# Kernel tuning notes

Measured on AMD Instinct MI355X. Metric: run time of the kernel, lower is better.

The kernel has to match this reference:

```python
import jax, jax.numpy as jnp
import numpy as np

B, P, T = 32, 196, 64
E = H = A = 512
V = 32000
L = 2  # num_layers


def _p(key, shape, scale=0.05):
    return jax.random.normal(key, shape, dtype=jnp.float32) * scale


def setup_inputs() -> dict:
    key = jax.random.key(0)
    ks = jax.random.split(key, 24)
    inp = {
        "encoder_out": jax.random.normal(ks[0], (B, P, E), dtype=jnp.float32),
        "captions": jax.random.randint(ks[1], (B, T), 0, V, dtype=jnp.int32),
        # embedding table (also tied fc weight)
        "emb_W": _p(ks[2], (V, E)),
        "fc_b": jnp.zeros((V,), jnp.float32),
        # attention
        "W_enc": _p(ks[3], (E, A)), "b_enc": jnp.zeros((A,), jnp.float32),
        "W_dec": _p(ks[4], (H, A)), "b_dec": jnp.zeros((A,), jnp.float32),
        "W_full": _p(ks[5], (A, 1)), "b_full": jnp.zeros((1,), jnp.float32),
        # LSTM layer 0 (input = 2E), layer 1 (input = H); PyTorch gate order i,f,g,o
        "Wih0": _p(ks[6], (4 * H, 2 * E)), "Whh0": _p(ks[7], (4 * H, H)),
        "bih0": jnp.zeros((4 * H,), jnp.float32), "bhh0": jnp.zeros((4 * H,), jnp.float32),
        "Wih1": _p(ks[8], (4 * H, H)), "Whh1": _p(ks[9], (4 * H, H)),
        "bih1": jnp.zeros((4 * H,), jnp.float32), "bhh1": jnp.zeros((4 * H,), jnp.float32),
        # init hidden/cell projections
        "W_init_h": _p(ks[10], (E, H * L)), "b_init_h": jnp.zeros((H * L,), jnp.float32),
        "W_init_c": _p(ks[11], (E, H * L)), "b_init_c": jnp.zeros((H * L,), jnp.float32),
    }
    return inp


def _lstm_cell(x, h, c, Wih, Whh, b):
    gates = x @ Wih.T + h @ Whh.T + b  # [B, 4H]
    i, f, g, o = jnp.split(gates, 4, axis=-1)
    c_new = jax.nn.sigmoid(f) * c + jax.nn.sigmoid(i) * jnp.tanh(g)
    h_new = jax.nn.sigmoid(o) * jnp.tanh(c_new)
    return h_new, c_new


def _forward(encoder_out, captions, emb_W, fc_b, W_enc, b_enc, W_dec, b_dec,
             W_full, b_full, Wih0, Whh0, bih0, bhh0, Wih1, Whh1, bih1, bhh1,
             W_init_h, b_init_h, W_init_c, b_init_c):
    # dropout is identity (eval mode)
    Bsz = encoder_out.shape[0]
    mean_enc = encoder_out.mean(axis=1)  # [B, E]
    # PyTorch: .view(num_layers, B, -1) on a [B, H*L] tensor -> flat reshape
    h = (mean_enc @ W_init_h + b_init_h).reshape(L, Bsz, H)
    c = (mean_enc @ W_init_c + b_init_c).reshape(L, Bsz, H)

    enc_att = encoder_out @ W_enc + b_enc  # [B, P, A] (timestep-invariant, hoisted)
    embs = emb_W[captions]  # [B, T, E]
    b0 = bih0 + bhh0
    b1 = bih1 + bhh1

    def step(carry, emb_t):
        h, c = carry  # each [L, B, H]
        att2 = h[-1] @ W_dec + b_dec  # [B, A]
        e = (jax.nn.relu(enc_att + att2[:, None, :]) @ W_full)[..., 0] + b_full[0]  # [B, P]
        alpha = jax.nn.softmax(e, axis=1)
        context = jnp.einsum('bp,bpe->be', alpha, encoder_out)  # [B, E]
        x = jnp.concatenate([emb_t, context], axis=-1)  # [B, 2E]
        h0, c0 = _lstm_cell(x, h[0], c[0], Wih0, Whh0, b0)
        h1, c1 = _lstm_cell(h0, h[1], c[1], Wih1, Whh1, b1)
        out = h1 @ emb_W.T + fc_b  # tied-weight projection [B, V]
        return (jnp.stack([h0, h1]), jnp.stack([c0, c1])), out

    (_, _), outs = jax.lax.scan(step, (h, c), jnp.swapaxes(embs, 0, 1))
    return jnp.swapaxes(outs, 0, 1)  # [B, T, V]


def reference(encoder_out, captions, emb_W, fc_b, W_enc, b_enc, W_dec, b_dec,
              W_full, b_full, Wih0, Whh0, bih0, bhh0, Wih1, Whh1, bih1, bhh1,
              W_init_h, b_init_h, W_init_c, b_init_c):
    return _forward(encoder_out, captions, emb_W, fc_b, W_enc, b_enc, W_dec, b_dec,
                    W_full, b_full, Wih0, Whh0, bih0, bhh0, Wih1, Whh1, bih1, bhh1,
                    W_init_h, b_init_h, W_init_c, b_init_c)
```

## Files before the change

### kernel.cpp

```cpp
#include <hip/hip_runtime.h>

typedef unsigned short u16;
typedef __attribute__((ext_vector_type(4))) float f32x4;
typedef __attribute__((ext_vector_type(2))) float f32x2;
typedef __attribute__((ext_vector_type(8))) short short8;

#define B_ 32
#define P_ 196
#define T_ 64
#define V_ 32000
#define SLABF 17408

#define AT_LOAD(p)     __hip_atomic_load((p), __ATOMIC_RELAXED, __HIP_MEMORY_SCOPE_AGENT)
#define AT_STORE(p,v)  __hip_atomic_store((p), (v), __ATOMIC_RELAXED, __HIP_MEMORY_SCOPE_AGENT)

__device__ __forceinline__ u16 f2bf(float x){
  unsigned int u = __float_as_uint(x);
  u += 0x7FFFu + ((u >> 16) & 1u);
  return (u16)(u >> 16);
}
__device__ __forceinline__ float bf2f(u16 x){
  return __uint_as_float(((unsigned int)x) << 16);
}
__device__ __forceinline__ float sigf(float x){ return 1.0f/(1.0f + __expf(-x)); }
__device__ __forceinline__ float tanhfast(float x){
  float e = __expf(-2.0f*fabsf(x));
  float t = (1.0f - e)/(1.0f + e);
  return x >= 0.0f ? t : -t;
}


__global__ __launch_bounds__(256) void k_cvt_bf16(const float* __restrict__ s,
                                                  u16* __restrict__ d, int n8){
  int i = blockIdx.x*256 + threadIdx.x;
  if (i >= n8) return;
  const f32x4* sp = (const f32x4*)(s + (size_t)i*8);
  f32x4 a = sp[0], b = sp[1];
  short8 v;
#pragma unroll
  for (int j=0;j<4;++j){ v[j] = (short)f2bf(a[j]); v[4+j] = (short)f2bf(b[j]); }
  *(short8*)(d + (size_t)i*8) = v;
}

__global__ __launch_bounds__(256) void k_wencT(const float* __restrict__ W, u16* __restrict__ WT){
  int tid = threadIdx.x;
  int kc = tid & 63, a = blockIdx.x*4 + (tid >> 6);
  short8 v;
#pragma unroll
  for (int j=0;j<8;++j) v[j] = (short)f2bf(W[(kc*8+j)*512 + a]);
  *(short8*)(WT + a*512 + kc*8) = v;
}

__global__ __launch_bounds__(256) void k_mean(const float* __restrict__ enc, float* __restrict__ mean){
  int b = blockIdx.x, tid = threadIdx.x;
  f32x2 acc; acc.x = 0.f; acc.y = 0.f;
  for (int p=0;p<P_;++p){
    f32x2 v = *(const f32x2*)(enc + ((size_t)(b*P_+p))*512 + tid*2);
    acc.x += v.x; acc.y += v.y;
  }
  acc.x *= (1.0f/196.0f); acc.y *= (1.0f/196.0f);
  *(f32x2*)(mean + b*512 + tid*2) = acc;
}

__global__ __launch_bounds__(256) void k_init_state(const float* __restrict__ mean,
    const float* __restrict__ Wh, const float* __restrict__ bh,
    const float* __restrict__ Wc, const float* __restrict__ bc,
    float* __restrict__ h0, float* __restrict__ h1,
    float* __restrict__ c0, float* __restrict__ c1){
  int bid = blockIdx.x;
  int which = bid >> 7, r = (bid >> 2) & 31, jg = bid & 3;
  const float* W = which ? Wc : Wh;
  const float* bb = which ? bc : bh;
  __shared__ float m[512];
  for (int i=threadIdx.x; i<512; i+=256) m[i] = mean[r*512 + i];
  __syncthreads();
  int j = jg*256 + threadIdx.x;
  float acc = bb[j];
  for (int e=0;e<512;++e) acc += m[e]*W[e*1024 + j];
  int l = r >> 4;
  int bb2 = ((r & 15) << 1) | (j >> 9);
  int hh = j & 511;
  float* dst = which ? (l ? c1 : c0) : (l ? h1 : h0);
  dst[bb2*512 + hh] = acc;
}

__global__ __launch_bounds__(256) void k_fuse_w(const float* __restrict__ Wih0,
    const float* __restrict__ Whh0, const float* __restrict__ Wih1,
    const float* __restrict__ Whh1, float* __restrict__ W0f, float* __restrict__ W1f){
  int r = blockIdx.x, tid = threadIdx.x;
  if (r < 2048){
    for (int k=tid; k<1536; k+=256)
      W0f[(size_t)r*1536+k] = (k<1024) ? Wih0[(size_t)r*1024+k] : Whh0[(size_t)r*512 + (k-1024)];
  } else {
    int r1 = r - 2048;
    for (int k=tid; k<1024; k+=256)
      W1f[(size_t)r1*1024+k] = (k<512) ? Wih1[(size_t)r1*512+k] : Whh1[(size_t)r1*512 + (k-512)];
  }
}

#define LDAP 40
__global__ __launch_bounds__(256) void k_gemm_bf16(
    const u16* __restrict__ A, const u16* __restrict__ Bm,
    const float* __restrict__ bias, float* __restrict__ C, int N){
  __shared__ __align__(16) u16 As[128*LDAP];
  __shared__ __align__(16) u16 Bs[128*LDAP];
  int tid = threadIdx.x, l = tid & 63, w = tid >> 6;
  int m0 = blockIdx.x * 128, n0 = blockIdx.y * 128;
  int wm = w >> 1, wn = w & 1;
  f32x4 acc[4][4];
#pragma unroll
  for (int a=0;a<4;++a)
#pragma unroll
    for (int b=0;b<4;++b) acc[a][b] = (f32x4)0.0f;
  int srow = tid >> 2, schunk = tid & 3;
  const u16* gA = A + (size_t)(m0 + srow)*512 + schunk*8;
  const u16* gB = Bm + (size_t)(n0 + srow)*512 + schunk*8;
  int lr = l & 15, lk = (l >> 4) * 8;
  for (int k0 = 0; k0 < 512; k0 += 32){
    short8 va0 = *(const short8*)(gA + k0);
    short8 va1 = *(const short8*)(gA + (size_t)64*512 + k0);
    short8 vb0 = *(const short8*)(gB + k0);
    short8 vb1 = *(const short8*)(gB + (size_t)64*512 + k0);
    __syncthreads();
    *(short8*)(As + srow*LDAP + schunk*8) = va0;
    *(short8*)(As + (64+srow)*LDAP + schunk*8) = va1;
    *(short8*)(Bs + srow*LDAP + schunk*8) = vb0;
    *(short8*)(Bs + (64+srow)*LDAP + schunk*8) = vb1;
    __syncthreads();
    short8 af[4], bfv[4];
#pragma unroll
    for (int mt=0; mt<4; ++mt) af[mt]  = *(const short8*)(As + (wm*64 + mt*16 + lr)*LDAP + lk);
#pragma unroll
    for (int nt=0; nt<4; ++nt) bfv[nt] = *(const short8*)(Bs + (wn*64 + nt*16 + lr)*LDAP + lk);
#pragma unroll
    for (int mt=0; mt<4; ++mt)
#pragma unroll
      for (int nt=0; nt<4; ++nt)
        acc[mt][nt] = __builtin_amdgcn_mfma_f32_16x16x32_bf16(af[mt], bfv[nt], acc[mt][nt], 0, 0, 0);
  }
#pragma unroll
  for (int mt=0; mt<4; ++mt){
    int row = m0 + wm*64 + mt*16 + ((l >> 4) << 2);
#pragma unroll
    for (int nt=0; nt<4; ++nt){
      int col = n0 + wn*64 + nt*16 + (l & 15);
      float bv = bias[col];
#pragma unroll
      for (int j=0;j<4;++j)
        C[(size_t)(row + j)*N + col] = acc[mt][nt][j] + bv;
    }
  }
}


struct RA {
  const float* enc; const int* caps; const float* embW;
  const u16* WdecBF; const float* bdec; const float* Wfull; const float* bfull;
  const u16* encattBF; const float* W0f; const float* W1f;
  const float* bih0; const float* bhh0; const float* bih1; const float* bhh1;
  float* h0g; float* h1g; float* att2g; float* ctxg;
  const float* c0init; const float* c1init;
  u16* h1_all; int* slots; int* go;
};

__device__ __forceinline__ void gbar(int* slots, int* go, int gen){
  __syncthreads();
  if (blockIdx.x == 0){
    int tid = threadIdx.x;
    if (tid >= 1 && tid < 256){
      while (AT_LOAD(&slots[tid]) < gen) __builtin_amdgcn_s_sleep(1);
    }
    __syncthreads();
    if (tid == 0) AT_STORE(go, gen);
  } else {
    if (threadIdx.x == 0){
      AT_STORE(&slots[blockIdx.x], gen);
      while (AT_LOAD(go) < gen) __builtin_amdgcn_s_sleep(1);
    }
    __syncthreads();
  }
  asm volatile("" ::: "memory");
}

__global__ __launch_bounds__(512) void k_recur(RA a){
  int bid = blockIdx.x, tid = threadIdx.x;
  int lane = tid & 63, wv = tid >> 6;
  __shared__ __align__(16) float w0s[12288];
  __shared__ __align__(16) float w1s[8192];
  __shared__ float red[2048];
  __shared__ float c0s[64], c1s[64];
  __shared__ float SinvS;
  __shared__ int capl[32];

  int xcd = bid & 7;
  int ab = xcd*4 + ((bid >> 3) & 3);
  int as = bid >> 5, c0col = as*64;
  int bb = tid >> 4, ksg = tid & 15;

  for (int idx = tid; idx < 12288; idx += 512){
    int r = idx / 1536, rem = idx - r*1536;
    int ch = rem >> 9, rem2 = rem & 511;
    int q = rem2 >> 6, rem3 = rem2 & 63;
    int ks = rem3 >> 2, e = rem3 & 3;
    int grow = (r >> 1)*512 + bid*2 + (r & 1);
    w0s[idx] = a.W0f[(size_t)grow*1536 + ch*512 + ks*32 + q*4 + e];
  }
  for (int idx = tid; idx < 8192; idx += 512){
    int r = idx >> 10, rem = idx & 1023;
    int ch = rem >> 9, rem2 = rem & 511;
    int q = rem2 >> 6, rem3 = rem2 & 63;
    int ks = rem3 >> 2, e = rem3 & 3;
    int grow = (r >> 1)*512 + bid*2 + (r & 1);
    w1s[idx] = a.W1f[(size_t)grow*1024 + ch*512 + ks*32 + q*4 + e];
  }
  if (tid < 64){
    int ci = tid >> 5, b = tid & 31, cell = bid*2 + ci;
    c0s[ci*32+b] = a.c0init[b*512 + cell];
    c1s[ci*32+b] = a.c1init[b*512 + cell];
  }
  __syncthreads();

  for (int t = 0; t < T_; ++t){
    const float* h1_rd = a.h1g + (size_t)t*SLABF;
    const float* h0_rd = a.h0g + (size_t)t*SLABF;
    float*       h0_wr = a.h0g + (size_t)(t+1)*SLABF;
    float*       h1_wr = a.h1g + (size_t)(t+1)*SLABF;
    float*       at_wr = a.att2g + (size_t)t*SLABF;
    const float* at_rd = at_wr;
    float*       cx_wr = a.ctxg + (size_t)t*SLABF;
    const float* cx_rd = cx_wr;
    int genb = t*4;

    {
      float* h1s = red; float* gp = red + 512;
      h1s[tid] = h1_rd[ab*512 + tid];
      __syncthreads();
      int c = lane, ksx = wv;
      float accp = 0.f;
      const u16* wpd = a.WdecBF + (size_t)(ksx*64)*512 + c0col + c;
#pragma unroll 8
      for (int i=0;i<64;++i) accp = fmaf(h1s[ksx*64+i], bf2f(wpd[(size_t)i*512]), accp);
      gp[ksx*64+c] = accp;
      __syncthreads();
      if (tid < 64){
        float s = a.bdec[c0col+tid];
#pragma unroll
        for (int k=0;k<8;++k) s += gp[k*64+tid];
        AT_STORE(&at_wr[ab*512 + c0col + tid], s);
      }
    }
    gbar(a.slots, a.go, genb+1);

    {
      float* att2s = red; float* gp3 = red + 512; float* alph = red + 1024;
      att2s[tid] = at_rd[ab*512 + tid];
      __syncthreads();
      float a2[8], wf[8];
#pragma unroll
      for (int j=0;j<8;++j){ a2[j] = att2s[lane*8+j]; wf[j] = a.Wfull[lane*8+j]; }
      float bf0 = a.bfull[0];
      int np = (wv < 4) ? 25 : 24;
      for (int i=0;i<np;++i){
        int p = wv + i*8;
        const u16* ep = a.encattBF + ((size_t)(ab*P_ + p))*512 + lane*8;
        short8 ev = *(const short8*)ep;
        float s = 0.f;
#pragma unroll
        for (int j=0;j<8;++j)
          s += fmaxf(bf2f((u16)ev[j]) + a2[j], 0.f) * wf[j];
#pragma unroll
        for (int o=32;o>=1;o>>=1) s += __shfl_xor(s, o);
        if (lane == 0) alph[p] = __expf(s + bf0);
      }
      __syncthreads();
      if (wv == 0){
        float v = 0.f;
#pragma unroll
        for (int i=0;i<4;++i){ int p = lane + 64*i; if (p < P_) v += alph[p]; }
#pragma unroll
        for (int o=32;o>=1;o>>=1) v += __shfl_xor(v, o);
        if (lane == 0) SinvS = 1.0f / v;
      }
      int c = lane, pk = wv;
      float accp = 0.f;
      for (int i=0;i<25;++i){
        int p = pk + 8*i;
        if (p < P_) accp = fmaf(alph[p], a.enc[((size_t)(ab*P_ + p))*512 + c0col + c], accp);
      }
      gp3[pk*64+c] = accp;
      __syncthreads();
      if (tid < 64){
        float s = 0.f;
#pragma unroll
        for (int k=0;k<8;++k) s += gp3[k*64+tid];
        AT_STORE(&cx_wr[ab*512 + c0col + tid], s * SinvS);
      }
    }
    gbar(a.slots, a.go, genb+2);

    {
      if (tid < 32) capl[tid] = a.caps[tid*T_ + t];
      __syncthreads();
      float acc[8];
#pragma unroll
      for (int r=0;r<8;++r) acc[r] = 0.f;
#pragma unroll
      for (int ch=0; ch<3; ++ch){
        const float* src;
        if (ch == 0)      src = a.embW + (size_t)capl[bb]*512 + ksg*32;
        else if (ch == 1) src = cx_rd + bb*512 + ksg*32;
        else              src = h0_rd + bb*512 + ksg*32;
        f32x4 x[8];
#pragma unroll
        for (int q=0;q<8;++q) x[q] = *(const f32x4*)(src + q*4);
        const float* wb = w0s + ch*512 + ksg*4;
#pragma unroll
        for (int q=0;q<8;++q){
          f32x4 xq = x[q];
#pragma unroll
          for (int r=0;r<8;++r){
            f32x4 w4 = *(const f32x4*)(wb + r*1536 + q*64);
            acc[r] = fmaf(xq.x,w4.x, fmaf(xq.y,w4.y, fmaf(xq.z,w4.z, fmaf(xq.w,w4.w, acc[r]))));
          }
        }
      }
#pragma unroll
      for (int r=0;r<8;++r){
        float v = acc[r];
        v += __shfl_xor(v,1); v += __shfl_xor(v,2); v += __shfl_xor(v,4); v += __shfl_xor(v,8);
        acc[r] = v;
      }
      if (ksg == 0){
#pragma unroll
        for (int ci=0;ci<2;++ci){
          int cell = bid*2 + ci;
          float gi = acc[0+ci] + a.bih0[cell]        + a.bhh0[cell];
          float gf = acc[2+ci] + a.bih0[512+cell]    + a.bhh0[512+cell];
          float gg = acc[4+ci] + a.bih0[1024+cell]   + a.bhh0[1024+cell];
          float go = acc[6+ci] + a.bih0[1536+cell]   + a.bhh0[1536+cell];
          float cp = c0s[ci*32+bb];
          float cn = sigf(gf)*cp + sigf(gi)*tanhfast(gg);
          float hn = sigf(go)*tanhfast(cn);
          c0s[ci*32+bb] = cn;
          AT_STORE(&h0_wr[bb*512 + cell], hn);
        }
      }
    }
    gbar(a.slots, a.go, genb+3);

    {
      float acc[8];
#pragma unroll
      for (int r=0;r<8;++r) acc[r] = 0.f;
#pragma unroll
      for (int ch=0; ch<2; ++ch){
        const float* src = (ch == 0) ? (h0_wr + bb*512 + ksg*32)
                                     : (h1_rd + bb*512 + ksg*32);
        f32x4 x[8];
#pragma unroll
        for (int q=0;q<8;++q) x[q] = *(const f32x4*)(src + q*4);
        const float* wb = w1s + ch*512 + ksg*4;
#pragma unroll
        for (int q=0;q<8;++q){
          f32x4 xq = x[q];
#pragma unroll
          for (int r=0;r<8;++r){
            f32x4 w4 = *(const f32x4*)(wb + r*1024 + q*64);
            acc[r] = fmaf(xq.x,w4.x, fmaf(xq.y,w4.y, fmaf(xq.z,w4.z, fmaf(xq.w,w4.w, acc[r]))));
          }
        }
      }
#pragma unroll
      for (int r=0;r<8;++r){
        float v = acc[r];
        v += __shfl_xor(v,1); v += __shfl_xor(v,2); v += __shfl_xor(v,4); v += __shfl_xor(v,8);
        acc[r] = v;
      }
      if (ksg == 0){
#pragma unroll
        for (int ci=0;ci<2;++ci){
          int cell = bid*2 + ci;
          float gi = acc[0+ci] + a.bih1[cell]        + a.bhh1[cell];
          float gf = acc[2+ci] + a.bih1[512+cell]    + a.bhh1[512+cell];
          float gg = acc[4+ci] + a.bih1[1024+cell]   + a.bhh1[1024+cell];
          float go = acc[6+ci] + a.bih1[1536+cell]   + a.bhh1[1536+cell];
          float cp = c1s[ci*32+bb];
          float cn = sigf(gf)*cp + sigf(gi)*tanhfast(gg);
          float hn = sigf(go)*tanhfast(cn);
          c1s[ci*32+bb] = cn;
          AT_STORE(&h1_wr[bb*512 + cell], hn);
          a.h1_all[((size_t)(bb*T_ + t))*512 + cell] = f2bf(hn);
        }
      }
    }
    gbar(a.slots, a.go, genb+4);
  }
}


extern "C" void kernel_launch(void* const* d_in, const int* in_sizes, int n_in,
                              void* d_out, int out_size, void* d_ws, size_t ws_size,
                              hipStream_t stream){
  const float* enc   = (const float*)d_in[0];
  const int*   caps  = (const int*)d_in[1];
  const float* embW  = (const float*)d_in[2];
  const float* fc_b  = (const float*)d_in[3];
  const float* Wenc  = (const float*)d_in[4];
  const float* benc  = (const float*)d_in[5];
  const float* Wdec  = (const float*)d_in[6];
  const float* bdec  = (const float*)d_in[7];
  const float* Wfull = (const float*)d_in[8];
  const float* bfull = (const float*)d_in[9];
  const float* Wih0  = (const float*)d_in[10];
  const float* Whh0  = (const float*)d_in[11];
  const float* bih0  = (const float*)d_in[12];
  const float* bhh0  = (const float*)d_in[13];
  const float* Wih1  = (const float*)d_in[14];
  const float* Whh1  = (const float*)d_in[15];
  const float* bih1  = (const float*)d_in[16];
  const float* bhh1  = (const float*)d_in[17];
  const float* Winh  = (const float*)d_in[18];
  const float* binh  = (const float*)d_in[19];
  const float* Winc  = (const float*)d_in[20];
  const float* binc  = (const float*)d_in[21];
  float* out = (float*)d_out;

  char* wsp = (char*)d_ws;
  size_t off = 0;
  auto alloc = [&](size_t bytes)->char*{
    char* p = wsp + off;
    off += (bytes + 255) & ~(size_t)255;
    return p;
  };
  u16*   A_enc    = (u16*)  alloc((size_t)6272*512*2);
  u16*   emb_bf   = (u16*)  alloc((size_t)V_*512*2);
  u16*   WencT    = (u16*)  alloc((size_t)512*512*2);
  u16*   WdecBF   = (u16*)  alloc((size_t)512*512*2);
  float* encatt   = (float*)alloc((size_t)6272*512*4);
  u16*   encattBF = (u16*)  alloc((size_t)6272*512*2);
  float* meanb    = (float*)alloc((size_t)32*512*4);
  float* W0f      = (float*)alloc((size_t)2048*1536*4);
  float* W1f      = (float*)alloc((size_t)2048*1024*4);
  float* h0g      = (float*)alloc((size_t)65*SLABF*4);
  float* h1g      = (float*)alloc((size_t)65*SLABF*4);
  float* att2g    = (float*)alloc((size_t)65*SLABF*4);
  float* ctxg     = (float*)alloc((size_t)65*SLABF*4);
  float* c0init   = (float*)alloc(32*512*4);
  float* c1init   = (float*)alloc(32*512*4);
  u16*   h1_all   = (u16*)  alloc((size_t)2048*512*2);
  int*   syncA    = (int*)  alloc(257*4);
  if (off > ws_size) return;
  int* slots = syncA; int* go = syncA + 256;

  hipMemsetAsync(syncA, 0, 257*4, stream);
  k_cvt_bf16<<<1568, 256, 0, stream>>>(enc, A_enc, 401408);
  k_cvt_bf16<<<8000, 256, 0, stream>>>(embW, emb_bf, 2048000);
  k_cvt_bf16<<<128, 256, 0, stream>>>(Wdec, WdecBF, 32768);
  k_wencT   <<<128, 256, 0, stream>>>(Wenc, WencT);
  k_mean    <<<32, 256, 0, stream>>>(enc, meanb);
  k_init_state<<<256, 256, 0, stream>>>(meanb, Winh, binh, Winc, binc,
                                        h0g, h1g, c0init, c1init);
  k_fuse_w<<<4096, 256, 0, stream>>>(Wih0, Whh0, Wih1, Whh1, W0f, W1f);
  k_gemm_bf16<<<dim3(49, 4), 256, 0, stream>>>(A_enc, WencT, benc, encatt, 512);
  k_cvt_bf16<<<1568, 256, 0, stream>>>(encatt, encattBF, 401408);

  RA ra;
  ra.enc = enc; ra.caps = caps; ra.embW = embW;
  ra.WdecBF = WdecBF; ra.bdec = bdec; ra.Wfull = Wfull; ra.bfull = bfull;
  ra.encattBF = encattBF; ra.W0f = W0f; ra.W1f = W1f;
  ra.bih0 = bih0; ra.bhh0 = bhh0; ra.bih1 = bih1; ra.bhh1 = bhh1;
  ra.h0g = h0g; ra.h1g = h1g; ra.att2g = att2g; ra.ctxg = ctxg;
  ra.c0init = c0init; ra.c1init = c1init;
  ra.h1_all = h1_all; ra.slots = slots; ra.go = go;
  void* kp[] = { &ra };
  hipLaunchCooperativeKernel((const void*)k_recur, dim3(256), dim3(512), kp, 0, stream);

  k_gemm_bf16<<<dim3(16, 250), 256, 0, stream>>>(h1_all, emb_bf, fc_b, out, V_);
}
```

Before: 2.447 ms.

## Pad barrier slots, add two-level release tree, prefetch embedding and h0 early

The grid barrier now spaces each block's arrival slot 128 bytes apart to avoid false sharing. Release becomes two levels: blocks 1-8 watch the master flag and re-publish it to per-XCD flags, which the other blocks poll. This spreads the polling load off a single cache line. Separately, the layer-0 embedding row and previous h0 are loaded into registers at the start of each step, ahead of the attention phases, so those loads are off the critical path after the barrier. This costs extra register pressure (64 floats live across the barriers) and an extra hop in the release path.

Measured after the change: 2.692 ms. 1.1x slower.

```diff
diff --git a/kernel.cpp b/kernel.cpp
--- a/kernel.cpp
+++ b/kernel.cpp
@@ -160,22 +160,28 @@
   const float* bih0; const float* bhh0; const float* bih1; const float* bhh1;
   float* h0g; float* h1g; float* att2g; float* ctxg;
   const float* c0init; const float* c1init;
-  u16* h1_all; int* slots; int* go;
+  u16* h1_all; int* sync;
 };
 
-__device__ __forceinline__ void gbar(int* slots, int* go, int gen){
+__device__ __forceinline__ void gbar(int* sync, int gen){
+  int* slots = sync; int* go = sync + 8192; int* goR = sync + 8224;
   __syncthreads();
-  if (blockIdx.x == 0){
-    int tid = threadIdx.x;
+  int tid = threadIdx.x, bid = blockIdx.x;
+  if (bid == 0){
     if (tid >= 1 && tid < 256){
-      while (AT_LOAD(&slots[tid]) < gen) __builtin_amdgcn_s_sleep(1);
+      while (AT_LOAD(&slots[tid*32]) < gen) __builtin_amdgcn_s_sleep(1);
     }
     __syncthreads();
     if (tid == 0) AT_STORE(go, gen);
   } else {
-    if (threadIdx.x == 0){
-      AT_STORE(&slots[blockIdx.x], gen);
-      while (AT_LOAD(go) < gen) __builtin_amdgcn_s_sleep(1);
+    if (tid == 0){
+      AT_STORE(&slots[bid*32], gen);
+      if (bid <= 8){
+        while (AT_LOAD(go) < gen) __builtin_amdgcn_s_sleep(1);
+        AT_STORE(&goR[(bid-1)*32], gen);
+      } else {
+        while (AT_LOAD(&goR[(bid & 7)*32]) < gen) __builtin_amdgcn_s_sleep(1);
+      }
     }
     __syncthreads();
   }
@@ -190,7 +196,6 @@
   __shared__ float red[2048];
   __shared__ float c0s[64], c1s[64];
   __shared__ float SinvS;
-  __shared__ int capl[32];
 
   int xcd = bid & 7;
   int ab = xcd*4 + ((bid >> 3) & 3);
@@ -230,6 +235,18 @@
     float*       cx_wr = a.ctxg + (size_t)t*SLABF;
     const float* cx_rd = cx_wr;
     int genb = t*4;
+
+    int cap = a.caps[bb*T_ + t];
+    f32x4 xe[8], xh[8];
+    {
+      const float* ep_ = a.embW + (size_t)cap*512 + ksg*32;
+      const float* hp_ = h0_rd + bb*512 + ksg*32;
+#pragma unroll
+      for (int q=0;q<8;++q){
+        xe[q] = *(const f32x4*)(ep_ + q*4);
+        xh[q] = *(const f32x4*)(hp_ + q*4);
+      }
+    }
 
     {
       float* h1s = red; float* gp = red + 512;
@@ -249,7 +266,7 @@
         AT_STORE(&at_wr[ab*512 + c0col + tid], s);
       }
     }
-    gbar(a.slots, a.go, genb+1);
+    gbar(a.sync, genb+1);
 
     {
       float* att2s = red; float* gp3 = red + 512; float* alph = red + 1024;
@@ -296,32 +313,44 @@
         AT_STORE(&cx_wr[ab*512 + c0col + tid], s * SinvS);
       }
     }
-    gbar(a.slots, a.go, genb+2);
+    gbar(a.sync, genb+2);
 
     {
-      if (tid < 32) capl[tid] = a.caps[tid*T_ + t];
-      __syncthreads();
       float acc[8];
 #pragma unroll
       for (int r=0;r<8;++r) acc[r] = 0.f;
-#pragma unroll
-      for (int ch=0; ch<3; ++ch){
-        const float* src;
-        if (ch == 0)      src = a.embW + (size_t)capl[bb]*512 + ksg*32;
-        else if (ch == 1) src = cx_rd + bb*512 + ksg*32;
-        else              src = h0_rd + bb*512 + ksg*32;
-        f32x4 x[8];
-#pragma unroll
-        for (int q=0;q<8;++q) x[q] = *(const f32x4*)(src + q*4);
-        const float* wb = w0s + ch*512 + ksg*4;
-#pragma unroll
-        for (int q=0;q<8;++q){
-          f32x4 xq = x[q];
-#pragma unroll
-          for (int r=0;r<8;++r){
-            f32x4 w4 = *(const f32x4*)(wb + r*1536 + q*64);
-            acc[r] = fmaf(xq.x,w4.x, fmaf(xq.y,w4.y, fmaf(xq.z,w4.z, fmaf(xq.w,w4.w, acc[r]))));
-          }
+      f32x4 xc[8];
+      {
+        const float* cs = cx_rd + bb*512 + ksg*32;
+#pragma unroll
+        for (int q=0;q<8;++q) xc[q] = *(const f32x4*)(cs + q*4);
+      }
+      const float* wb = w0s + ksg*4;
+#pragma unroll
+      for (int q=0;q<8;++q){
+        f32x4 xq = xe[q];
+#pragma unroll
+        for (int r=0;r<8;++r){
+          f32x4 w4 = *(const f32x4*)(wb + r*1536 + q*64);
+          acc[r] = fmaf(xq.x,w4.x, fmaf(xq.y,w4.y, fmaf(xq.z,w4.z, fmaf(xq.w,w4.w, acc[r]))));
+        }
+      }
+#pragma unroll
+      for (int q=0;q<8;++q){
+        f32x4 xq = xc[q];
+#pragma unroll
+        for (int r=0;r<8;++r){
+          f32x4 w4 = *(const f32x4*)(wb + r*1536 + 512 + q*64);
+          acc[r] = fmaf(xq.x,w4.x, fmaf(xq.y,w4.y, fmaf(xq.z,w4.z, fmaf(xq.w,w4.w, acc[r]))));
+        }
+      }
+#pragma unroll
+      for (int q=0;q<8;++q){
+        f32x4 xq = xh[q];
+#pragma unroll
+        for (int r=0;r<8;++r){
+          f32x4 w4 = *(const f32x4*)(wb + r*1536 + 1024 + q*64);
+          acc[r] = fmaf(xq.x,w4.x, fmaf(xq.y,w4.y, fmaf(xq.z,w4.z, fmaf(xq.w,w4.w, acc[r]))));
         }
       }
 #pragma unroll
@@ -346,7 +375,7 @@
         }
       }
     }
-    gbar(a.slots, a.go, genb+3);
+    gbar(a.sync, genb+3);
 
     {
       float acc[8];
@@ -393,7 +422,7 @@
         }
       }
     }
-    gbar(a.slots, a.go, genb+4);
+    gbar(a.sync, genb+4);
   }
 }
 
@@ -448,11 +477,10 @@
   float* c0init   = (float*)alloc(32*512*4);
   float* c1init   = (float*)alloc(32*512*4);
   u16*   h1_all   = (u16*)  alloc((size_t)2048*512*2);
-  int*   syncA    = (int*)  alloc(257*4);
+  int*   syncA    = (int*)  alloc(8480*4);
   if (off > ws_size) return;
-  int* slots = syncA; int* go = syncA + 256;
-
-  hipMemsetAsync(syncA, 0, 257*4, stream);
+
+  hipMemsetAsync(syncA, 0, 8480*4, stream);
   k_cvt_bf16<<<1568, 256, 0, stream>>>(enc, A_enc, 401408);
   k_cvt_bf16<<<8000, 256, 0, stream>>>(embW, emb_bf, 2048000);
   k_cvt_bf16<<<128, 256, 0, stream>>>(Wdec, WdecBF, 32768);
@@ -471,7 +499,7 @@
   ra.bih0 = bih0; ra.bhh0 = bhh0; ra.bih1 = bih1; ra.bhh1 = bhh1;
   ra.h0g = h0g; ra.h1g = h1g; ra.att2g = att2g; ra.ctxg = ctxg;
   ra.c0init = c0init; ra.c1init = c1init;
-  ra.h1_all = h1_all; ra.slots = slots; ra.go = go;
+  ra.h1_all = h1_all; ra.sync = syncA;
   void* kp[] = { &ra };
   hipLaunchCooperativeKernel((const void*)k_recur, dim3(256), dim3(512), kp, 0, stream);
 
```
